# Optimization experiments

Hardware: AMD Instinct MI355X
Metric: run time of the kernel (lower is better)

Reference implementation:

```python
import jax, jax.numpy as jnp
import numpy as np

B, N, F_, H = 4, 2048, 1024, 16
DH = F_ // H
SCALE = F_ / 19.5  # module uses feats/19.5, not sqrt(head_dim)


def setup_inputs() -> dict:
    key = jax.random.key(0)
    ks = jax.random.split(key, 9)
    s = 1.0 / np.sqrt(F_)
    return {
        "x": jax.random.normal(ks[0], (B, N, F_), jnp.float32),
        "Wq": jax.random.normal(ks[1], (F_, F_), jnp.float32) * s,
        "bq": jax.random.normal(ks[2], (F_,), jnp.float32) * s,
        "Wk": jax.random.normal(ks[3], (F_, F_), jnp.float32) * s,
        "bk": jax.random.normal(ks[4], (F_,), jnp.float32) * s,
        "Wv": jax.random.normal(ks[5], (F_, F_), jnp.float32) * s,
        "bv": jax.random.normal(ks[6], (F_,), jnp.float32) * s,
        "Wo": jax.random.normal(ks[7], (F_, F_), jnp.float32) * s,
        "bo": jax.random.normal(ks[8], (F_,), jnp.float32) * s,
    }


def reference(x, Wq, bq, Wk, bk, Wv, bv, Wo, bo):
    b, n, f = x.shape
    # torch Linear: x @ W.T + b; then view(b,n,h,dh).transpose(1,2) -> bhnd
    def proj(W, bias):
        return (x @ W.T + bias).reshape(b, n, H, DH).transpose(0, 2, 1, 3)

    q = proj(Wq, bq)  # [b,h,n,dh]
    k = proj(Wk, bk)
    v = proj(Wv, bv)
    score = jax.nn.softmax(jnp.einsum("bhif,bhjf->bhij", q, k) / SCALE, axis=-1)
    attn = jnp.einsum("bhij,bhjf->bihf", score, v)  # [b,n,h,dh]
    o = attn.reshape(b, n, f) @ Wo.T + bo  # dropout p=0.0 -> identity
    return o
```

## Files before the change

kernel.cpp:

```cpp
#include <hip/hip_runtime.h>
#include <stdint.h>

typedef unsigned short u16;
typedef __bf16 bf16x8 __attribute__((ext_vector_type(8)));
typedef float f32x4 __attribute__((ext_vector_type(4)));

#define QSCALE (19.5f/1024.0f * 1.44269504088896340736f)
#define EXPMAGIC 12599162.0f

__device__ __forceinline__ u16 f2bf(float f){
  uint32_t u = __float_as_uint(f);
  return (u16)((u + 0x7FFFu + ((u >> 16) & 1u)) >> 16);
}

__device__ __forceinline__ uint64_t cvt4(float4 f){
  union{ u16 u[4]; uint64_t v; } pk;
  pk.u[0]=f2bf(f.x); pk.u[1]=f2bf(f.y); pk.u[2]=f2bf(f.z); pk.u[3]=f2bf(f.w);
  return pk.v;
}

#define GLD_LDS16(g,l) __builtin_amdgcn_global_load_lds( \
    (const __attribute__((address_space(1))) void*)(g),  \
    (__attribute__((address_space(3))) void*)(l), 16, 0, 0)

__global__ __launch_bounds__(256) void k_prep(
    const float4* __restrict__ x,  const float4* __restrict__ Wq,
    const float4* __restrict__ Wk, const float4* __restrict__ Wv,
    const float4* __restrict__ Wo,
    const float4* __restrict__ bq, const float4* __restrict__ bk, const float4* __restrict__ bv,
    uint64_t* __restrict__ xb, uint64_t* __restrict__ wqkv, uint64_t* __restrict__ wob,
    float4* __restrict__ bqkv)
{
  const int NX = 2097152, NW = 262144;
  const int total = NX + 4*NW + 768;
  int i = blockIdx.x*256 + threadIdx.x;
  const int stride = gridDim.x*256;
  for (; i < total; i += stride){
    if (i < NX)             xb[i] = cvt4(x[i]);
    else if (i < NX+NW)     { int j = i-NX;      wqkv[j]      = cvt4(Wq[j]); }
    else if (i < NX+2*NW)   { int j = i-NX-NW;   wqkv[NW+j]   = cvt4(Wk[j]); }
    else if (i < NX+3*NW)   { int j = i-NX-2*NW; wqkv[2*NW+j] = cvt4(Wv[j]); }
    else if (i < NX+4*NW)   { int j = i-NX-3*NW; wob[j]       = cvt4(Wo[j]); }
    else {
      int j = i - NX - 4*NW;
      bqkv[j] = (j < 256) ? bq[j] : (j < 512 ? bk[j-256] : bv[j-512]);
    }
  }
}

template<int MODE>
__global__ __launch_bounds__(256) void gemm_bt(
    const u16* __restrict__ A, const u16* __restrict__ Bw,
    const float* __restrict__ bias, float* __restrict__ Cout,
    u16* __restrict__ q_ws, u16* __restrict__ k_ws, u16* __restrict__ v_ws)
{
  __shared__ u16 lds[3*8192];
  const int tid  = threadIdx.x;
  const int w    = tid >> 6, lane = tid & 63;
  const int wr   = w >> 1,  wc   = w & 1;
  const int g    = lane >> 4, c16 = lane & 15;
  const int nt   = blockIdx.x, mt = blockIdx.y;
  const size_t arow0 = (size_t)mt * 128, brow0 = (size_t)nt * 128;

  f32x4 acc[4][4] = {};

  const int srow  = w*16 + (lane >> 2);
  const int schk  = ((lane & 3) ^ ((lane >> 3) & 3)) * 8;
  const u16* gA = A  + (arow0 + srow)*1024 + schk;
  const u16* gB = Bw + (brow0 + srow)*1024 + schk;

  u16* ldsA0 = &lds[w*512];
  u16* ldsB0 = &lds[4096 + w*512];

  const int rswz = (g ^ ((c16 >> 1) & 3)) * 8;
  const int abase = (wr*64 + c16)*32 + rswz;
  const int bbase = 4096 + (wc*64 + c16)*32 + rswz;

#define GSTAGE(B2) do{ \
    GLD_LDS16(gA,          ldsA0 + (B2)*8192); \
    GLD_LDS16(gA + 65536,  ldsA0 + (B2)*8192 + 2048); \
    GLD_LDS16(gB,          ldsB0 + (B2)*8192); \
    GLD_LDS16(gB + 65536,  ldsB0 + (B2)*8192 + 2048); \
    gA += 32; gB += 32; \
  }while(0)

#define GBODY(B, STG, VMW) do{ \
    if (STG) GSTAGE(((B)+2)%3); \
    bf16x8 af[4], bfr[4]; \
    _Pragma("unroll") \
    for (int m = 0; m < 4; m++) \
      af[m]  = __builtin_bit_cast(bf16x8, *(const uint4*)(&lds[(B)*8192 + abase + m*512])); \
    _Pragma("unroll") \
    for (int n = 0; n < 4; n++) \
      bfr[n] = __builtin_bit_cast(bf16x8, *(const uint4*)(&lds[(B)*8192 + bbase + n*512])); \
    __builtin_amdgcn_s_setprio(1); \
    _Pragma("unroll") \
    for (int m = 0; m < 4; m++) \
      _Pragma("unroll") \
      for (int n = 0; n < 4; n++) \
        acc[m][n] = __builtin_amdgcn_mfma_f32_16x16x32_bf16(af[m], bfr[n], acc[m][n], 0, 0, 0); \
    __builtin_amdgcn_s_setprio(0); \
    if ((VMW) == 4){ asm volatile("s_waitcnt vmcnt(4)" ::: "memory"); __builtin_amdgcn_s_barrier(); } \
    else if ((VMW) == 0){ asm volatile("s_waitcnt vmcnt(0)" ::: "memory"); __builtin_amdgcn_s_barrier(); } \
  }while(0)

  GSTAGE(0); GSTAGE(1);
  asm volatile("s_waitcnt vmcnt(4)" ::: "memory");
  __builtin_amdgcn_s_barrier();

  #pragma unroll 1
  for (int rr = 0; rr < 10; rr++){
    GBODY(0, 1, 4);
    GBODY(1, 1, 4);
    GBODY(2, 1, 4);
  }
  GBODY(0, 0, 0);
  GBODY(1, 0, -1);

#undef GBODY
#undef GSTAGE

  #pragma unroll
  for (int m = 0; m < 4; m++){
    const size_t i0 = arow0 + wr*64 + m*16 + g*4;
    #pragma unroll
    for (int n = 0; n < 4; n++){
      const int o = (int)brow0 + wc*64 + n*16 + c16;
      const float bias_v = bias[o];
      if (MODE == 0){
        const int proj = o >> 10, wi = o & 1023, hh = wi >> 6, dd = wi & 63;
        if (proj < 2){
          u16* base = (proj == 0) ? q_ws : k_ws;
          const float sc = (proj == 0) ? QSCALE : 1.0f;
          #pragma unroll
          for (int r = 0; r < 4; r++){
            const size_t i = i0 + r;
            const size_t bb = i >> 11, nn = i & 2047;
            base[((bb*16 + hh)*2048 + nn)*64 + dd] = f2bf((acc[m][n][r] + bias_v)*sc);
          }
        } else {
          const size_t bb = i0 >> 11, nn = i0 & 2047;
          union{ u16 u[4]; uint64_t v; } pk;
          #pragma unroll
          for (int r = 0; r < 4; r++) pk.u[r] = f2bf(acc[m][n][r] + bias_v);
          *reinterpret_cast<uint64_t*>(v_ws + ((bb*16 + hh)*64 + dd)*2048 + nn) = pk.v;
        }
      } else {
        #pragma unroll
        for (int r = 0; r < 4; r++)
          Cout[(i0 + r)*1024 + o] = acc[m][n][r] + bias_v;
      }
    }
  }
}

__global__ __launch_bounds__(256, 2) void attn_k(
    const u16* __restrict__ Q, const u16* __restrict__ Kb, const u16* __restrict__ Vt,
    u16* __restrict__ O)
{
  __shared__ u16 lds[3*8192];
  const int tid = threadIdx.x, w = tid >> 6, lane = tid & 63;
  const int g = lane >> 4, l16 = lane & 15;

  const int f   = ((blockIdx.x & 7) << 6) | (blockIdx.x >> 3);
  const int qt_ = f & 7, bh = f >> 3;
  const int b = bh >> 4, h = bh & 15;
  const size_t hb = (size_t)bh * 2048 * 64;

  const int qrow0 = qt_*256 + w*64 + l16;
  bf16x8 qf[4][2];
  #pragma unroll
  for (int qt = 0; qt < 4; qt++)
    #pragma unroll
    for (int kc = 0; kc < 2; kc++)
      qf[qt][kc] = __builtin_bit_cast(bf16x8,
        *(const uint4*)(Q + hb + (size_t)(qrow0 + qt*16)*64 + kc*32 + g*8));

  f32x4 acc[4][4] = {};
  f32x4 lacc[4] = {};

  union{ u16 u[8]; bf16x8 f; } one_;
  #pragma unroll
  for (int i = 0; i < 8; i++) one_.u[i] = 0x3F80;
  const bf16x8 onesv = one_.f;

  const int srowL = w*8 + (lane >> 3);
  const int schunk = ((lane & 7) ^ ((lane >> 3) & 7)) * 8;
  const u16* gKs = Kb + hb + (size_t)srowL*64   + schunk;
  const u16* gVs = Vt + hb + (size_t)srowL*2048 + schunk;

  u16* ldsK0 = &lds[w*512];
  u16* ldsV0 = &lds[4096 + w*512];

  const int kb0 = l16*64 + (g ^ (l16 & 7))*8;
  const int kb1 = kb0 ^ 32;
  const int vswz = l16 & 7, vlo = (g & 1)*4, vg2 = g >> 1;
  int vb[2][2];
  #pragma unroll
  for (int p = 0; p < 2; p++)
    #pragma unroll
    for (int pc = 0; pc < 2; pc++)
      vb[p][pc] = l16*64 + (((p*4 + pc*2 + vg2) ^ vswz) << 3) + vlo;

#define STAGE_T(B2) do{ \
    GLD_LDS16(gKs,          ldsK0 + (B2)*8192); \
    GLD_LDS16(gKs + 2048,   ldsK0 + (B2)*8192 + 2048); \
    GLD_LDS16(gVs,          ldsV0 + (B2)*8192); \
    GLD_LDS16(gVs + 65536,  ldsV0 + (B2)*8192 + 2048); \
    gKs += 4096; gVs += 64; \
  }while(0)

#define BODY_T(B, STG, VMW) do{ \
    if (STG) STAGE_T(((B)+2)%3); \
    _Pragma("unroll") \
    for (int p = 0; p < 2; p++){ \
      uint32_t pklo[2][4], pkhi[2][4]; \
      _Pragma("unroll") \
      for (int jh = 0; jh < 2; jh++){ \
        const int jt = p*2 + jh; \
        bf16x8 kf0 = __builtin_bit_cast(bf16x8, *(const uint4*)(&lds[(B)*8192 + jt*1024] + kb0)); \
        bf16x8 kf1 = __builtin_bit_cast(bf16x8, *(const uint4*)(&lds[(B)*8192 + jt*1024] + kb1)); \
        _Pragma("unroll") \
        for (int qt = 0; qt < 4; qt++){ \
          f32x4 st = {0.f,0.f,0.f,0.f}; \
          st = __builtin_amdgcn_mfma_f32_16x16x32_bf16(kf0, qf[qt][0], st, 0, 0, 0); \
          st = __builtin_amdgcn_mfma_f32_16x16x32_bf16(kf1, qf[qt][1], st, 0, 0, 0); \
          const uint32_t y0 = __float_as_uint(fmaf(st[0], 128.f, EXPMAGIC)); \
          const uint32_t y1 = __float_as_uint(fmaf(st[1], 128.f, EXPMAGIC)); \
          const uint32_t y2 = __float_as_uint(fmaf(st[2], 128.f, EXPMAGIC)); \
          const uint32_t y3 = __float_as_uint(fmaf(st[3], 128.f, EXPMAGIC)); \
          pklo[jh][qt] = __builtin_amdgcn_perm(y1, y0, 0x05040100u); \
          pkhi[jh][qt] = __builtin_amdgcn_perm(y3, y2, 0x05040100u); \
        } \
      } \
      union { uint32_t u[4]; bf16x8 f; } pf[4]; \
      _Pragma("unroll") \
      for (int qt = 0; qt < 4; qt++){ \
        pf[qt].u[0] = pklo[0][qt]; pf[qt].u[1] = pkhi[0][qt]; \
        pf[qt].u[2] = pklo[1][qt]; pf[qt].u[3] = pkhi[1][qt]; \
      } \
      __builtin_amdgcn_s_setprio(1); \
      _Pragma("unroll") \
      for (int qt = 0; qt < 4; qt++) \
        lacc[qt] = __builtin_amdgcn_mfma_f32_16x16x32_bf16(onesv, pf[qt].f, lacc[qt], 0, 0, 0); \
      _Pragma("unroll") \
      for (int dt = 0; dt < 4; dt++){ \
        union { uint64_t v[2]; bf16x8 f; } vf; \
        vf.v[0] = *(const uint64_t*)(&lds[(B)*8192 + 4096 + dt*1024] + vb[p][0]); \
        vf.v[1] = *(const uint64_t*)(&lds[(B)*8192 + 4096 + dt*1024] + vb[p][1]); \
        _Pragma("unroll") \
        for (int qt = 0; qt < 4; qt++) \
          acc[dt][qt] = __builtin_amdgcn_mfma_f32_16x16x32_bf16(vf.f, pf[qt].f, acc[dt][qt], 0, 0, 0); \
      } \
      __builtin_amdgcn_s_setprio(0); \
    } \
    if ((VMW) == 4){ asm volatile("s_waitcnt vmcnt(4)" ::: "memory"); __builtin_amdgcn_s_barrier(); } \
    else if ((VMW) == 0){ asm volatile("s_waitcnt vmcnt(0)" ::: "memory"); __builtin_amdgcn_s_barrier(); } \
  }while(0)

  STAGE_T(0); STAGE_T(1);
  asm volatile("s_waitcnt vmcnt(4)" ::: "memory");
  __builtin_amdgcn_s_barrier();

  #pragma unroll 1
  for (int rr = 0; rr < 10; rr++){
    BODY_T(0, 1, 4);
    BODY_T(1, 1, 4);
    BODY_T(2, 1, 4);
  }
  BODY_T(0, 0, 0);
  BODY_T(1, 0, -1);

#undef BODY_T
#undef STAGE_T

  float inv[4];
  #pragma unroll
  for (int qt = 0; qt < 4; qt++) inv[qt] = 1.f / lacc[qt][0];

  #pragma unroll
  for (int qt = 0; qt < 4; qt++){
    const size_t ob = (((size_t)(b*2048 + qrow0 + qt*16))*16 + h)*64;
    #pragma unroll
    for (int dt = 0; dt < 4; dt++){
      union{ u16 u[4]; uint64_t v; } pkk;
      #pragma unroll
      for (int r = 0; r < 4; r++) pkk.u[r] = f2bf(acc[dt][qt][r] * inv[qt]);
      *reinterpret_cast<uint64_t*>(O + ob + dt*16 + g*4) = pkk.v;
    }
  }
}

extern "C" void kernel_launch(void* const* d_in, const int* in_sizes, int n_in,
                              void* d_out, int out_size, void* d_ws, size_t ws_size,
                              hipStream_t stream)
{
  const float* x  = (const float*)d_in[0];
  const float* Wq = (const float*)d_in[1];
  const float* bq = (const float*)d_in[2];
  const float* Wk = (const float*)d_in[3];
  const float* bk = (const float*)d_in[4];
  const float* Wv = (const float*)d_in[5];
  const float* bv = (const float*)d_in[6];
  const float* Wo = (const float*)d_in[7];
  const float* bo = (const float*)d_in[8];
  float* out = (float*)d_out;

  char* ws = (char*)d_ws;
  size_t off = 0;
  auto bump = [&](size_t bytes){ size_t o = off; off = (off + bytes + 255) & ~(size_t)255; return o; };
  u16*  xb   = (u16*)  (ws + bump(8388608ull*2));
  u16*  wqkv = (u16*)  (ws + bump(3145728ull*2));
  u16*  wob  = (u16*)  (ws + bump(1048576ull*2));
  float* bqkv= (float*)(ws + bump(3072ull*4));
  u16*  qws  = (u16*)  (ws + bump(8388608ull*2));
  u16*  kws  = (u16*)  (ws + bump(8388608ull*2));
  u16*  vws  = (u16*)  (ws + bump(8388608ull*2));
  u16*  att  = (u16*)  (ws + bump(8388608ull*2));

  k_prep<<<2048, 256, 0, stream>>>(
      (const float4*)x, (const float4*)Wq, (const float4*)Wk, (const float4*)Wv, (const float4*)Wo,
      (const float4*)bq, (const float4*)bk, (const float4*)bv,
      (uint64_t*)xb, (uint64_t*)wqkv, (uint64_t*)wob, (float4*)bqkv);

  gemm_bt<0><<<dim3(24, 64), 256, 0, stream>>>(xb, wqkv, bqkv, nullptr, qws, kws, vws);
  attn_k<<<512, 256, 0, stream>>>(qws, kws, vws, att);
  gemm_bt<1><<<dim3(8, 64), 256, 0, stream>>>(att, wob, bo, out, nullptr, nullptr, nullptr);
}
```

Before: 163.0 us.

## Use 256x256 tiles for the QKV projection GEMM

Adds a dedicated QKV projection kernel that computes 256x256 output tiles per block. Each wave holds an 8x8 grid of MFMA accumulators, and the kernel keeps a 3-stage LDS pipeline at double the stage size. The larger tile raises operand reuse per LDS load and halves the global traffic per output, at the cost of much higher register pressure (256 accumulator floats per lane) and one block per CU. The grid drops to 384 blocks, which is only about 1.5 waves on the device and may leave CUs idle in the tail. The output GEMM is split out into its own non-templated kernel and is otherwise unchanged.

```diff
diff --git a/kernel.cpp b/kernel.cpp
--- a/kernel.cpp
+++ b/kernel.cpp
@@ -48,11 +48,108 @@
   }
 }
 
-template<int MODE>
-__global__ __launch_bounds__(256) void gemm_bt(
+__global__ __launch_bounds__(256, 1) void gemm256w(
     const u16* __restrict__ A, const u16* __restrict__ Bw,
-    const float* __restrict__ bias, float* __restrict__ Cout,
+    const float* __restrict__ bias,
     u16* __restrict__ q_ws, u16* __restrict__ k_ws, u16* __restrict__ v_ws)
+{
+  __shared__ u16 lds[3*16384];
+  const int tid  = threadIdx.x;
+  const int w    = tid >> 6, lane = tid & 63;
+  const int wr   = w >> 1,  wc   = w & 1;
+  const int g    = lane >> 4, c16 = lane & 15;
+  const int nt   = blockIdx.x, mt = blockIdx.y;
+  const size_t arow0 = (size_t)mt * 256, brow0 = (size_t)nt * 256;
+
+  f32x4 acc[8][8] = {};
+
+  const int schk = ((tid & 3) ^ ((tid >> 3) & 3)) * 8;
+  const u16* gA = A  + (arow0 + (tid >> 2))*1024 + schk;
+  const u16* gB = Bw + (brow0 + (tid >> 2))*1024 + schk;
+
+  const int rswz = (g ^ ((c16 >> 1) & 3)) * 8;
+  const int abase = (wr*128 + c16)*32 + rswz;
+  const int bbase = 8192 + (wc*128 + c16)*32 + rswz;
+
+#define GSTAGE(B2) do{ \
+    GLD_LDS16(gA,           &lds[(B2)*16384 +         tid*8]); \
+    GLD_LDS16(gA +  65536,  &lds[(B2)*16384 +  2048 + tid*8]); \
+    GLD_LDS16(gA + 131072,  &lds[(B2)*16384 +  4096 + tid*8]); \
+    GLD_LDS16(gA + 196608,  &lds[(B2)*16384 +  6144 + tid*8]); \
+    GLD_LDS16(gB,           &lds[(B2)*16384 +  8192 + tid*8]); \
+    GLD_LDS16(gB +  65536,  &lds[(B2)*16384 + 10240 + tid*8]); \
+    GLD_LDS16(gB + 131072,  &lds[(B2)*16384 + 12288 + tid*8]); \
+    GLD_LDS16(gB + 196608,  &lds[(B2)*16384 + 14336 + tid*8]); \
+    gA += 32; gB += 32; \
+  }while(0)
+
+#define GBODY(B, STG, VMW) do{ \
+    if (STG) GSTAGE(((B)+2)%3); \
+    bf16x8 af[8], bfr[8]; \
+    _Pragma("unroll") \
+    for (int m = 0; m < 8; m++) \
+      af[m]  = __builtin_bit_cast(bf16x8, *(const uint4*)(&lds[(B)*16384 + abase + m*512])); \
+    _Pragma("unroll") \
+    for (int n = 0; n < 8; n++) \
+      bfr[n] = __builtin_bit_cast(bf16x8, *(const uint4*)(&lds[(B)*16384 + bbase + n*512])); \
+    __builtin_amdgcn_s_setprio(1); \
+    _Pragma("unroll") \
+    for (int m = 0; m < 8; m++) \
+      _Pragma("unroll") \
+      for (int n = 0; n < 8; n++) \
+        acc[m][n] = __builtin_amdgcn_mfma_f32_16x16x32_bf16(af[m], bfr[n], acc[m][n], 0, 0, 0); \
+    __builtin_amdgcn_s_setprio(0); \
+    if ((VMW) == 8){ asm volatile("s_waitcnt vmcnt(8)" ::: "memory"); __builtin_amdgcn_s_barrier(); } \
+    else if ((VMW) == 0){ asm volatile("s_waitcnt vmcnt(0)" ::: "memory"); __builtin_amdgcn_s_barrier(); } \
+  }while(0)
+
+  GSTAGE(0); GSTAGE(1);
+  asm volatile("s_waitcnt vmcnt(8)" ::: "memory");
+  __builtin_amdgcn_s_barrier();
+
+  #pragma unroll 1
+  for (int rr = 0; rr < 10; rr++){
+    GBODY(0, 1, 8);
+    GBODY(1, 1, 8);
+    GBODY(2, 1, 8);
+  }
+  GBODY(0, 0, 0);
+  GBODY(1, 0, -1);
+
+#undef GBODY
+#undef GSTAGE
+
+  #pragma unroll
+  for (int m = 0; m < 8; m++){
+    const size_t i0 = arow0 + wr*128 + m*16 + g*4;
+    #pragma unroll
+    for (int n = 0; n < 8; n++){
+      const int o = (int)brow0 + wc*128 + n*16 + c16;
+      const float bias_v = bias[o];
+      const int proj = o >> 10, wi = o & 1023, hh = wi >> 6, dd = wi & 63;
+      if (proj < 2){
+        u16* base = (proj == 0) ? q_ws : k_ws;
+        const float sc = (proj == 0) ? QSCALE : 1.0f;
+        #pragma unroll
+        for (int r = 0; r < 4; r++){
+          const size_t i = i0 + r;
+          const size_t bb = i >> 11, nn = i & 2047;
+          base[((bb*16 + hh)*2048 + nn)*64 + dd] = f2bf((acc[m][n][r] + bias_v)*sc);
+        }
+      } else {
+        const size_t bb = i0 >> 11, nn = i0 & 2047;
+        union{ u16 u[4]; uint64_t v; } pk;
+        #pragma unroll
+        for (int r = 0; r < 4; r++) pk.u[r] = f2bf(acc[m][n][r] + bias_v);
+        *reinterpret_cast<uint64_t*>(v_ws + ((bb*16 + hh)*64 + dd)*2048 + nn) = pk.v;
+      }
+    }
+  }
+}
+
+__global__ __launch_bounds__(256) void gemm_bt1(
+    const u16* __restrict__ A, const u16* __restrict__ Bw,
+    const float* __restrict__ bias, float* __restrict__ Cout)
 {
   __shared__ u16 lds[3*8192];
   const int tid  = threadIdx.x;
@@ -127,29 +224,9 @@
     for (int n = 0; n < 4; n++){
       const int o = (int)brow0 + wc*64 + n*16 + c16;
       const float bias_v = bias[o];
-      if (MODE == 0){
-        const int proj = o >> 10, wi = o & 1023, hh = wi >> 6, dd = wi & 63;
-        if (proj < 2){
-          u16* base = (proj == 0) ? q_ws : k_ws;
-          const float sc = (proj == 0) ? QSCALE : 1.0f;
-          #pragma unroll
-          for (int r = 0; r < 4; r++){
-            const size_t i = i0 + r;
-            const size_t bb = i >> 11, nn = i & 2047;
-            base[((bb*16 + hh)*2048 + nn)*64 + dd] = f2bf((acc[m][n][r] + bias_v)*sc);
-          }
-        } else {
-          const size_t bb = i0 >> 11, nn = i0 & 2047;
-          union{ u16 u[4]; uint64_t v; } pk;
-          #pragma unroll
-          for (int r = 0; r < 4; r++) pk.u[r] = f2bf(acc[m][n][r] + bias_v);
-          *reinterpret_cast<uint64_t*>(v_ws + ((bb*16 + hh)*64 + dd)*2048 + nn) = pk.v;
-        }
-      } else {
-        #pragma unroll
-        for (int r = 0; r < 4; r++)
-          Cout[(i0 + r)*1024 + o] = acc[m][n][r] + bias_v;
-      }
+      #pragma unroll
+      for (int r = 0; r < 4; r++)
+        Cout[(i0 + r)*1024 + o] = acc[m][n][r] + bias_v;
     }
   }
 }
@@ -323,7 +400,7 @@
       (const float4*)bq, (const float4*)bk, (const float4*)bv,
       (uint64_t*)xb, (uint64_t*)wqkv, (uint64_t*)wob, (float4*)bqkv);
 
-  gemm_bt<0><<<dim3(24, 64), 256, 0, stream>>>(xb, wqkv, bqkv, nullptr, qws, kws, vws);
+  gemm256w<<<dim3(12, 32), 256, 0, stream>>>(xb, wqkv, bqkv, qws, kws, vws);
   attn_k<<<512, 256, 0, stream>>>(qws, kws, vws, att);
-  gemm_bt<1><<<dim3(8, 64), 256, 0, stream>>>(att, wob, bo, out, nullptr, nullptr, nullptr);
-}
+  gemm_bt1<<<dim3(8, 64), 256, 0, stream>>>(att, wob, bo, out);
+}
```

Measured after the change: 172.4 us. +5.8%, slower.

## Widen GEMM tiles to 128x256 with 512 threads and pair-buffer attention stages

Applied to the files above, without the earlier changes.

The projection GEMMs now use 128x256 output tiles computed by 8 waves (512 threads), so each A tile loaded into LDS is reused across twice as many output columns. Each thread issues three direct-to-LDS loads per stage. The attention kernel moves from a 3-stage ring to 4 LDS buffers processed in pairs, which halves the number of barriers but waits for vmcnt(0) at each sync. The trade-offs are fewer GEMM blocks (768 and 256), which means weaker wave-level occupancy balance, and more LDS per attention block, which may limit residency.

```diff
diff --git a/kernel.cpp b/kernel.cpp
--- a/kernel.cpp
+++ b/kernel.cpp
@@ -49,38 +49,33 @@
 }
 
 template<int MODE>
-__global__ __launch_bounds__(256) void gemm_bt(
+__global__ __launch_bounds__(512) void gemm128x256(
     const u16* __restrict__ A, const u16* __restrict__ Bw,
     const float* __restrict__ bias, float* __restrict__ Cout,
     u16* __restrict__ q_ws, u16* __restrict__ k_ws, u16* __restrict__ v_ws)
 {
-  __shared__ u16 lds[3*8192];
+  __shared__ u16 lds[3*12288];
   const int tid  = threadIdx.x;
   const int w    = tid >> 6, lane = tid & 63;
-  const int wr   = w >> 1,  wc   = w & 1;
+  const int wr   = w >> 2,  wc   = w & 3;
   const int g    = lane >> 4, c16 = lane & 15;
   const int nt   = blockIdx.x, mt = blockIdx.y;
-  const size_t arow0 = (size_t)mt * 128, brow0 = (size_t)nt * 128;
+  const size_t arow0 = (size_t)mt * 128, brow0 = (size_t)nt * 256;
 
   f32x4 acc[4][4] = {};
 
-  const int srow  = w*16 + (lane >> 2);
-  const int schk  = ((lane & 3) ^ ((lane >> 3) & 3)) * 8;
-  const u16* gA = A  + (arow0 + srow)*1024 + schk;
-  const u16* gB = Bw + (brow0 + srow)*1024 + schk;
-
-  u16* ldsA0 = &lds[w*512];
-  u16* ldsB0 = &lds[4096 + w*512];
+  const int schk = ((tid & 3) ^ ((tid >> 3) & 3)) * 8;
+  const u16* gA = A  + (arow0 + (tid >> 2))*1024 + schk;
+  const u16* gB = Bw + (brow0 + (tid >> 2))*1024 + schk;
 
   const int rswz = (g ^ ((c16 >> 1) & 3)) * 8;
   const int abase = (wr*64 + c16)*32 + rswz;
   const int bbase = 4096 + (wc*64 + c16)*32 + rswz;
 
 #define GSTAGE(B2) do{ \
-    GLD_LDS16(gA,          ldsA0 + (B2)*8192); \
-    GLD_LDS16(gA + 65536,  ldsA0 + (B2)*8192 + 2048); \
-    GLD_LDS16(gB,          ldsB0 + (B2)*8192); \
-    GLD_LDS16(gB + 65536,  ldsB0 + (B2)*8192 + 2048); \
+    GLD_LDS16(gA,           &lds[(B2)*12288 +        tid*8]); \
+    GLD_LDS16(gB,           &lds[(B2)*12288 + 4096 + tid*8]); \
+    GLD_LDS16(gB + 131072,  &lds[(B2)*12288 + 8192 + tid*8]); \
     gA += 32; gB += 32; \
   }while(0)
 
@@ -89,10 +84,10 @@
     bf16x8 af[4], bfr[4]; \
     _Pragma("unroll") \
     for (int m = 0; m < 4; m++) \
-      af[m]  = __builtin_bit_cast(bf16x8, *(const uint4*)(&lds[(B)*8192 + abase + m*512])); \
+      af[m]  = __builtin_bit_cast(bf16x8, *(const uint4*)(&lds[(B)*12288 + abase + m*512])); \
     _Pragma("unroll") \
     for (int n = 0; n < 4; n++) \
-      bfr[n] = __builtin_bit_cast(bf16x8, *(const uint4*)(&lds[(B)*8192 + bbase + n*512])); \
+      bfr[n] = __builtin_bit_cast(bf16x8, *(const uint4*)(&lds[(B)*12288 + bbase + n*512])); \
     __builtin_amdgcn_s_setprio(1); \
     _Pragma("unroll") \
     for (int m = 0; m < 4; m++) \
@@ -100,19 +95,19 @@
       for (int n = 0; n < 4; n++) \
         acc[m][n] = __builtin_amdgcn_mfma_f32_16x16x32_bf16(af[m], bfr[n], acc[m][n], 0, 0, 0); \
     __builtin_amdgcn_s_setprio(0); \
-    if ((VMW) == 4){ asm volatile("s_waitcnt vmcnt(4)" ::: "memory"); __builtin_amdgcn_s_barrier(); } \
+    if ((VMW) == 3){ asm volatile("s_waitcnt vmcnt(3)" ::: "memory"); __builtin_amdgcn_s_barrier(); } \
     else if ((VMW) == 0){ asm volatile("s_waitcnt vmcnt(0)" ::: "memory"); __builtin_amdgcn_s_barrier(); } \
   }while(0)
 
   GSTAGE(0); GSTAGE(1);
-  asm volatile("s_waitcnt vmcnt(4)" ::: "memory");
+  asm volatile("s_waitcnt vmcnt(3)" ::: "memory");
   __builtin_amdgcn_s_barrier();
 
   #pragma unroll 1
   for (int rr = 0; rr < 10; rr++){
-    GBODY(0, 1, 4);
-    GBODY(1, 1, 4);
-    GBODY(2, 1, 4);
+    GBODY(0, 1, 3);
+    GBODY(1, 1, 3);
+    GBODY(2, 1, 3);
   }
   GBODY(0, 0, 0);
   GBODY(1, 0, -1);
@@ -158,7 +153,7 @@
     const u16* __restrict__ Q, const u16* __restrict__ Kb, const u16* __restrict__ Vt,
     u16* __restrict__ O)
 {
-  __shared__ u16 lds[3*8192];
+  __shared__ u16 lds[4*8192];
   const int tid = threadIdx.x, w = tid >> 6, lane = tid & 63;
   const int g = lane >> 4, l16 = lane & 15;
 
@@ -210,8 +205,7 @@
     gKs += 4096; gVs += 64; \
   }while(0)
 
-#define BODY_T(B, STG, VMW) do{ \
-    if (STG) STAGE_T(((B)+2)%3); \
+#define TILE_T(B) do{ \
     _Pragma("unroll") \
     for (int p = 0; p < 2; p++){ \
       uint32_t pklo[2][4], pkhi[2][4]; \
@@ -254,24 +248,29 @@
       } \
       __builtin_amdgcn_s_setprio(0); \
     } \
-    if ((VMW) == 4){ asm volatile("s_waitcnt vmcnt(4)" ::: "memory"); __builtin_amdgcn_s_barrier(); } \
-    else if ((VMW) == 0){ asm volatile("s_waitcnt vmcnt(0)" ::: "memory"); __builtin_amdgcn_s_barrier(); } \
+  }while(0)
+
+#define PAIR_T(B0, B1, STG, SYNC) do{ \
+    if (STG){ STAGE_T((B0)^2); STAGE_T((B1)^2); } \
+    TILE_T(B0); \
+    TILE_T(B1); \
+    if (SYNC){ asm volatile("s_waitcnt vmcnt(0)" ::: "memory"); __builtin_amdgcn_s_barrier(); } \
   }while(0)
 
   STAGE_T(0); STAGE_T(1);
-  asm volatile("s_waitcnt vmcnt(4)" ::: "memory");
+  asm volatile("s_waitcnt vmcnt(0)" ::: "memory");
   __builtin_amdgcn_s_barrier();
 
   #pragma unroll 1
-  for (int rr = 0; rr < 10; rr++){
-    BODY_T(0, 1, 4);
-    BODY_T(1, 1, 4);
-    BODY_T(2, 1, 4);
-  }
-  BODY_T(0, 0, 0);
-  BODY_T(1, 0, -1);
-
-#undef BODY_T
+  for (int rr = 0; rr < 7; rr++){
+    PAIR_T(0, 1, 1, 1);
+    PAIR_T(2, 3, 1, 1);
+  }
+  PAIR_T(0, 1, 1, 1);
+  PAIR_T(2, 3, 0, 0);
+
+#undef PAIR_T
+#undef TILE_T
 #undef STAGE_T
 
   float inv[4];
@@ -323,7 +322,7 @@
       (const float4*)bq, (const float4*)bk, (const float4*)bv,
       (uint64_t*)xb, (uint64_t*)wqkv, (uint64_t*)wob, (float4*)bqkv);
 
-  gemm_bt<0><<<dim3(24, 64), 256, 0, stream>>>(xb, wqkv, bqkv, nullptr, qws, kws, vws);
+  gemm128x256<0><<<dim3(12, 64), 512, 0, stream>>>(xb, wqkv, bqkv, nullptr, qws, kws, vws);
   attn_k<<<512, 256, 0, stream>>>(qws, kws, vws, att);
-  gemm_bt<1><<<dim3(8, 64), 256, 0, stream>>>(att, wob, bo, out, nullptr, nullptr, nullptr);
-}
+  gemm128x256<1><<<dim3(4, 64), 512, 0, stream>>>(att, wob, bo, out, nullptr, nullptr, nullptr);
+}
```

After: 156.1 us. -4.2%, faster.
